# Performance work log

Measured on AMD Instinct MI355X. Metric: run time of the kernel, lower is better.

## Reference

```python
import jax, jax.numpy as jnp
import numpy as np

H = 64; W = 64; WS = 8; SS = 4; NH = 8; C = 256; IM = 4


def _rel_pos_index(ws: int) -> np.ndarray:
    coords = np.stack(np.meshgrid(np.arange(ws), np.arange(ws), indexing='ij'), axis=0).reshape(2, -1)
    rel = (coords[:, :, None] - coords[:, None, :]).transpose(1, 2, 0)
    rel[:, :, 0] += ws - 1
    rel[:, :, 1] += ws - 1
    rel[:, :, 0] *= 2 * ws - 1
    return rel.sum(-1).astype(np.int64)  # (ws*ws, ws*ws)


def _shift_mask(h: int, w: int, ws: int, ss: int) -> np.ndarray:
    img = np.zeros((h, w), np.float32)
    sl = (slice(0, -ws), slice(-ws, -ss), slice(-ss, None))
    cnt = 0
    for hs in sl:
        for wsl in sl:
            img[hs, wsl] = cnt
            cnt += 1
    mw = img.reshape(h // ws, ws, w // ws, ws).transpose(0, 2, 1, 3).reshape(-1, ws * ws)
    am = mw[:, None, :] - mw[:, :, None]
    return np.where(am != 0, -100.0, 0.0).astype(np.float32)  # (nW, n, n)


def setup_inputs() -> dict:
    key = jax.random.key(0)
    ks = jax.random.split(key, 16)
    s = 0.02
    d_ff = C * IM
    n_rel = (2 * WS - 1) ** 2
    return {
        'hidden_states': jax.random.normal(ks[0], (32, H * W, C), jnp.float32),
        'ln1_g': jnp.ones((C,), jnp.float32),
        'ln1_b': jnp.zeros((C,), jnp.float32),
        'wq': jax.random.normal(ks[1], (C, C), jnp.float32) * s,
        'bq': jnp.zeros((C,), jnp.float32),
        'wk': jax.random.normal(ks[2], (C, C), jnp.float32) * s,
        'bk': jnp.zeros((C,), jnp.float32),
        'wv': jax.random.normal(ks[3], (C, C), jnp.float32) * s,
        'bv': jnp.zeros((C,), jnp.float32),
        'bias_table': jax.random.normal(ks[4], (n_rel, NH), jnp.float32) * s,
        'wo': jax.random.normal(ks[5], (C, C), jnp.float32) * s,
        'bo': jnp.zeros((C,), jnp.float32),
        'ln2_g': jnp.ones((C,), jnp.float32),
        'ln2_b': jnp.zeros((C,), jnp.float32),
        'w1': jax.random.normal(ks[6], (C, d_ff), jnp.float32) * s,
        'b1': jnp.zeros((d_ff,), jnp.float32),
        'w2': jax.random.normal(ks[7], (d_ff, C), jnp.float32) * s,
        'b2': jnp.zeros((C,), jnp.float32),
    }


def _layernorm(x, g, b):
    m = x.mean(-1, keepdims=True)
    v = ((x - m) ** 2).mean(-1, keepdims=True)
    return (x - m) * jax.lax.rsqrt(v + 1e-5) * g + b


def reference(hidden_states, ln1_g, ln1_b, wq, bq, wk, bk, wv, bv, bias_table,
              wo, bo, ln2_g, ln2_b, w1, b1, w2, b2):
    B = hidden_states.shape[0]
    n = WS * WS
    hd = C // NH
    scale = hd ** -0.5
    nhw, nww = H // WS, W // WS
    nW = nhw * nww
    rpi = jnp.asarray(_rel_pos_index(WS))        # (n, n) int
    mask = jnp.asarray(_shift_mask(H, W, WS, SS))  # (nW, n, n)

    shortcut = hidden_states
    x = _layernorm(hidden_states, ln1_g, ln1_b).reshape(B, H, W, C)
    # cyclic shift
    x = jnp.roll(x, (-SS, -SS), axis=(1, 2))
    # window partition -> (B*nW, n, C)
    x = x.reshape(B, nhw, WS, nww, WS, C).transpose(0, 1, 3, 2, 4, 5).reshape(B * nW, n, C)

    q = (x @ wq + bq).reshape(B * nW, n, NH, hd).transpose(0, 2, 1, 3)
    k = (x @ wk + bk).reshape(B * nW, n, NH, hd).transpose(0, 2, 1, 3)
    v = (x @ wv + bv).reshape(B * nW, n, NH, hd).transpose(0, 2, 1, 3)

    attn = jnp.einsum('whnd,whmd->whnm', q, k) * scale  # (B*nW, NH, n, n)
    bias = bias_table[rpi.reshape(-1)].reshape(n, n, NH).transpose(2, 0, 1)
    attn = attn + bias[None]
    attn = attn.reshape(B, nW, NH, n, n) + mask[None, :, None]
    attn = jax.nn.softmax(attn.reshape(B * nW, NH, n, n), axis=-1)

    out = jnp.einsum('whnm,whmd->whnd', attn, v).transpose(0, 2, 1, 3).reshape(B * nW, n, C)
    out = out @ wo + bo
    # window reverse
    out = out.reshape(B, nhw, nww, WS, WS, C).transpose(0, 1, 3, 2, 4, 5).reshape(B, H, W, C)
    out = jnp.roll(out, (SS, SS), axis=(1, 2)).reshape(B, H * W, C)

    hs = shortcut + out
    y = _layernorm(hs, ln2_g, ln2_b)
    y = jax.nn.gelu(y @ w1 + b1, approximate=False)
    y = y @ w2 + b2
    return hs + y
```

## Files before the change

kernel.cpp:

```cpp
#include <hip/hip_runtime.h>
#include <hip/hip_bf16.h>
#include <math.h>

typedef unsigned short u16;
typedef __attribute__((ext_vector_type(8))) short bf16x8;
typedef __attribute__((ext_vector_type(8))) unsigned short u16x8;
typedef __attribute__((ext_vector_type(4))) float f32x4;

#define MFMA_BF16 __builtin_amdgcn_mfma_f32_16x16x32_bf16

__device__ __forceinline__ u16 f2bf(float f){
  union { float f; unsigned u; } v; v.f = f;
  unsigned r = v.u + 0x7FFFu + ((v.u >> 16) & 1u);
  return (u16)(r >> 16);
}

__device__ __forceinline__ void gll16(const void* g, void* l){
  __builtin_amdgcn_global_load_lds(
      (const __attribute__((address_space(1))) unsigned int*)g,
      (__attribute__((address_space(3))) unsigned int*)l, 16, 0, 0);
}

__global__ void k_concat_bias(const float* __restrict__ a, const float* __restrict__ b,
                              const float* __restrict__ c, float* __restrict__ o){
  int i = threadIdx.x;
  o[i] = i < 256 ? a[i] : (i < 512 ? b[i-256] : c[i-512]);
}

__global__ __launch_bounds__(256) void k_wfrag(const float* __restrict__ W, u16* __restrict__ F,
                                               int K, int N){
  int idx = blockIdx.x*256 + threadIdx.x;
  int nks = K >> 5;
  int per_n16 = nks << 9;
  int n16 = idx / per_n16; int rem = idx - n16*per_n16;
  int ks = rem >> 9, l8 = rem & 511, lane = l8 >> 3, j = l8 & 7;
  int k = ks*32 + ((lane >> 4) << 3) + j;
  int n = (n16 << 4) + (lane & 15);
  F[idx] = f2bf(W[(size_t)k*N + n]);
}

__global__ __launch_bounds__(256) void k_fragw(const float* __restrict__ wq, const float* __restrict__ wk,
                                               const float* __restrict__ wv, u16* __restrict__ fragW){
  int idx = blockIdx.x*256 + threadIdx.x;
  int j = idx & 7, lane = (idx >> 3) & 63, nj = (idx >> 9) & 1;
  int ks = (idx >> 10) & 7, h = (idx >> 13) & 7, type = idx >> 16;
  const float* w = type == 0 ? wq : (type == 1 ? wk : wv);
  int k = ks*32 + 8*(lane >> 4) + j;
  int n = h*32 + nj*16 + (lane & 15);
  fragW[idx] = f2bf(w[(size_t)k*256 + n]);
}

__global__ __launch_bounds__(256) void k_bias(const float* __restrict__ btab, float* __restrict__ fb){
  int idx = blockIdx.x*256 + threadIdx.x;
  int nj = idx & 3, lr = (idx >> 2) & 15, m = (idx >> 6) & 63, hh = (idx >> 12) & 7, cls = idx >> 15;
  int n = nj*16 + lr;
  int r1=m>>3, c1=m&7, r2=n>>3, c2=n&7;
  float bv = btab[((r1-r2+7)*15 + (c1-c2+7))*8 + hh];
  int whe = cls>>1, wwe = cls&1;
  int a1 = (whe ? (r1<4?1:2) : 0)*3 + (wwe ? (c1<4?1:2) : 0);
  int a2 = (whe ? (r2<4?1:2) : 0)*3 + (wwe ? (c2<4?1:2) : 0);
  fb[idx] = bv + ((a1!=a2) ? -100.f : 0.f);
}

__global__ __launch_bounds__(1024) void k_fattn(const float* __restrict__ hidden,
    const float* __restrict__ g1, const float* __restrict__ b1f,
    const u16* __restrict__ fragW, const float* __restrict__ bqkv,
    const float* __restrict__ fb, const u16* __restrict__ woF,
    const float* __restrict__ bo, const float* __restrict__ g2,
    const float* __restrict__ b2v,
    float* __restrict__ hs_out, u16* __restrict__ y2)
{
  __shared__ __align__(16) u16 lds[75776];
  int tid = threadIdx.x, lane = tid & 63, wid = tid >> 6;
  int lg = lane >> 4, lr = lane & 15;
  int h = wid >> 1, s = wid & 1;
  int gw = blockIdx.x;
  int bi = gw >> 6, win = gw & 63, wh = win >> 3, wwi = win & 7;

  {
    int t = wid*4 + (lane >> 4);
    int j = lane & 15;
    int hh_ = (wh*8 + (t >> 3) + 4) & 63;
    int ww_ = (wwi*8 + (t & 7) + 4) & 63;
    const float4* row = (const float4*)(hidden + ((size_t)bi*4096 + hh_*64 + ww_)*256) + j*4;
    float4 v[4]; float sm = 0.f, sq = 0.f;
#pragma unroll
    for (int i=0;i<4;i++){
      v[i] = row[i];
      sm += v[i].x+v[i].y+v[i].z+v[i].w;
      sq += v[i].x*v[i].x+v[i].y*v[i].y+v[i].z*v[i].z+v[i].w*v[i].w;
    }
    sm += __shfl_xor(sm,1); sq += __shfl_xor(sq,1);
    sm += __shfl_xor(sm,2); sq += __shfl_xor(sq,2);
    sm += __shfl_xor(sm,4); sq += __shfl_xor(sq,4);
    sm += __shfl_xor(sm,8); sq += __shfl_xor(sq,8);
    float mean = sm*(1.f/256.f);
    float inv = rsqrtf(sq*(1.f/256.f) - mean*mean + 1e-5f);
    const float4* gg = (const float4*)g1 + j*4;
    const float4* bb = (const float4*)b1f + j*4;
#pragma unroll
    for (int i2=0;i2<2;i2++){
      float4 a0=v[2*i2], a1=v[2*i2+1];
      float4 g0=gg[2*i2], g1_=gg[2*i2+1];
      float4 b0=bb[2*i2], b1_=bb[2*i2+1];
      u16x8 pk;
      pk[0]=f2bf((a0.x-mean)*inv*g0.x+b0.x); pk[1]=f2bf((a0.y-mean)*inv*g0.y+b0.y);
      pk[2]=f2bf((a0.z-mean)*inv*g0.z+b0.z); pk[3]=f2bf((a0.w-mean)*inv*g0.w+b0.w);
      pk[4]=f2bf((a1.x-mean)*inv*g1_.x+b1_.x); pk[5]=f2bf((a1.y-mean)*inv*g1_.y+b1_.y);
      pk[6]=f2bf((a1.z-mean)*inv*g1_.z+b1_.z); pk[7]=f2bf((a1.w-mean)*inv*g1_.w+b1_.w);
      int c = (j*2 + i2) ^ (t & 7);
      *(u16x8*)(&lds[t*256 + c*8]) = pk;
    }
  }
  __syncthreads();

  f32x4 qa[2][2]={}, ka[2][2]={}, va[2][2]={};
  __builtin_amdgcn_s_setprio(1);
#pragma unroll
  for (int ks=0; ks<8; ks++){
    bf16x8 af[2];
#pragma unroll
    for (int mi=0;mi<2;mi++){
      int tok = 32*s + mi*16 + lr;
      af[mi] = *(const bf16x8*)(&lds[tok*256 + (((ks*4+lg) ^ (tok&7))*8)]);
    }
    const u16* fq = fragW + ((((size_t)h)*8 + ks)*2)*512 + lane*8;
#pragma unroll
    for (int nj=0;nj<2;nj++){
      bf16x8 bq_ = *(const bf16x8*)(fq + nj*512);
      bf16x8 bk_ = *(const bf16x8*)(fq + 65536 + nj*512);
      bf16x8 bv_ = *(const bf16x8*)(fq + 131072 + nj*512);
#pragma unroll
      for (int mi=0;mi<2;mi++){
        qa[mi][nj] = MFMA_BF16(af[mi], bq_, qa[mi][nj], 0,0,0);
        ka[mi][nj] = MFMA_BF16(af[mi], bk_, ka[mi][nj], 0,0,0);
        va[mi][nj] = MFMA_BF16(af[mi], bv_, va[mi][nj], 0,0,0);
      }
    }
  }
  __builtin_amdgcn_s_setprio(0);

  u16* hb  = &lds[16384 + h*7424];
  u16* k_h = hb;
  u16* v_h = hb + 2560;
  u16* q_s = hb + 4864 + s*1280;
  const float scale = 0.1767766952966369f;
#pragma unroll
  for (int mi=0;mi<2;mi++)
#pragma unroll
  for (int nj=0;nj<2;nj++){
    int dim = nj*16+lr;
    float bq_ = bqkv[h*32+dim], bk_ = bqkv[256+h*32+dim], bv_ = bqkv[512+h*32+dim];
#pragma unroll
    for (int r=0;r<4;r++){
      int tokl = mi*16+4*lg+r;
      q_s[tokl*40+dim] = f2bf((qa[mi][nj][r]+bq_)*scale);
      k_h[(32*s+tokl)*40+dim] = f2bf(ka[mi][nj][r]+bk_);
    }
    ushort4 vp;
    vp.x = f2bf(va[mi][nj][0]+bv_); vp.y = f2bf(va[mi][nj][1]+bv_);
    vp.z = f2bf(va[mi][nj][2]+bv_); vp.w = f2bf(va[mi][nj][3]+bv_);
    *(ushort4*)(&v_h[dim*72 + 32*s + mi*16 + 4*lg]) = vp;
  }
  __syncthreads();

  bf16x8 qf[2], kf[4];
#pragma unroll
  for (int i=0;i<2;i++)
    qf[i] = *(const bf16x8*)(&q_s[(i*16+lr)*40 + 8*lg]);
#pragma unroll
  for (int i=0;i<4;i++)
    kf[i] = *(const bf16x8*)(&k_h[(i*16+lr)*40 + 8*lg]);
  f32x4 acc[2][4] = {};
#pragma unroll
  for (int mi=0;mi<2;mi++)
#pragma unroll
  for (int nj=0;nj<4;nj++)
    acc[mi][nj] = MFMA_BF16(qf[mi], kf[nj], acc[mi][nj], 0,0,0);

  int cls = ((wh==7) ? 2 : 0) | ((wwi==7) ? 1 : 0);
  const float4* fb4 = (const float4*)(fb + (((size_t)cls*8 + h) << 12));
#pragma unroll
  for (int mi=0;mi<2;mi++)
#pragma unroll
  for (int r=0;r<4;r++){
    int m = 32*s + mi*16 + 4*lg + r;
    float4 bv4 = fb4[m*16 + lr];
#pragma unroll
    for (int nj=0;nj<4;nj++)
      acc[mi][nj][r] += bv4[nj];
  }
#pragma unroll
  for (int mi=0;mi<2;mi++)
#pragma unroll
  for (int r=0;r<4;r++){
    float mx = fmaxf(fmaxf(acc[mi][0][r], acc[mi][1][r]), fmaxf(acc[mi][2][r], acc[mi][3][r]));
    for (int off=1; off<16; off<<=1) mx = fmaxf(mx, __shfl_xor(mx, off));
    float sum = 0.f;
#pragma unroll
    for (int nj=0;nj<4;nj++){ float e = __expf(acc[mi][nj][r]-mx); acc[mi][nj][r]=e; sum+=e; }
    for (int off=1; off<16; off<<=1) sum += __shfl_xor(sum, off);
    float inv = 1.f/sum;
#pragma unroll
    for (int nj=0;nj<4;nj++) acc[mi][nj][r] *= inv;
  }

  __syncthreads();

  u16* P_s = s ? hb : (hb + 4864);
#pragma unroll
  for (int mi=0;mi<2;mi++)
#pragma unroll
  for (int nj=0;nj<4;nj++)
#pragma unroll
  for (int r=0;r<4;r++)
    P_s[(mi*16+4*lg+r)*72 + nj*16 + lr] = f2bf(acc[mi][nj][r]);

  f32x4 acc2[2][2] = {};
#pragma unroll
  for (int ks=0; ks<2; ks++){
    bf16x8 vf0 = *(const bf16x8*)(&v_h[(lr)*72 + ks*32 + 8*lg]);
    bf16x8 vf1 = *(const bf16x8*)(&v_h[(16+lr)*72 + ks*32 + 8*lg]);
#pragma unroll
    for (int mi=0;mi<2;mi++){
      bf16x8 pf = *(const bf16x8*)(&P_s[(mi*16+lr)*72 + ks*32 + 8*lg]);
      acc2[mi][0] = MFMA_BF16(pf, vf0, acc2[mi][0], 0,0,0);
      acc2[mi][1] = MFMA_BF16(pf, vf1, acc2[mi][1], 0,0,0);
    }
  }

#pragma unroll
  for (int mi=0;mi<2;mi++)
#pragma unroll
  for (int nt=0;nt<2;nt++)
#pragma unroll
  for (int r=0;r<4;r++){
    int row = 32*s + mi*16 + 4*lg + r;
    int chunk = (4*h + 2*nt + (lr>>3)) ^ (row & 7);
    lds[row*256 + chunk*8 + (lr&7)] = f2bf(acc2[mi][nt][r]);
  }
  __syncthreads();

  f32x4 po[2][2] = {};
  __builtin_amdgcn_s_setprio(1);
#pragma unroll
  for (int ks=0; ks<8; ks++){
    bf16x8 af2[2];
#pragma unroll
    for (int mi=0;mi<2;mi++){
      int row = 32*s + mi*16 + lr;
      af2[mi] = *(const bf16x8*)(&lds[row*256 + (((ks*4+lg) ^ (row&7))*8)]);
    }
#pragma unroll
    for (int nj=0;nj<2;nj++){
      bf16x8 bw = *(const bf16x8*)(woF + (((size_t)(2*h+nj))*8 + ks)*512 + lane*8);
#pragma unroll
      for (int mi=0;mi<2;mi++)
        po[mi][nj] = MFMA_BF16(af2[mi], bw, po[mi][nj], 0,0,0);
    }
  }
  __builtin_amdgcn_s_setprio(0);

  float* part_s = (float*)&lds[16384];
  float* part_q = (float*)&lds[16384 + 1024];
  float bov[2], g2v[2], b2vv[2];
#pragma unroll
  for (int nj=0;nj<2;nj++){
    int n = 32*h + nj*16 + lr;
    bov[nj] = bo[n]; g2v[nj] = g2[n]; b2vv[nj] = b2v[n];
  }
#pragma unroll
  for (int mi=0;mi<2;mi++)
#pragma unroll
  for (int r=0;r<4;r++){
    int p = 32*s + mi*16 + 4*lg + r;
    int hh_ = (wh*8 + (p >> 3) + 4) & 63;
    int ww_ = (wwi*8 + (p & 7) + 4) & 63;
    size_t base = ((size_t)bi*4096 + hh_*64 + ww_)*256;
    float ls = 0.f, lq = 0.f;
#pragma unroll
    for (int nj=0;nj<2;nj++){
      int n = 32*h + nj*16 + lr;
      float v = po[mi][nj][r] + bov[nj] + hidden[base + n];
      hs_out[base + n] = v;
      po[mi][nj][r] = v;
      ls += v; lq += v*v;
    }
    ls += __shfl_xor(ls,1); lq += __shfl_xor(lq,1);
    ls += __shfl_xor(ls,2); lq += __shfl_xor(lq,2);
    ls += __shfl_xor(ls,4); lq += __shfl_xor(lq,4);
    ls += __shfl_xor(ls,8); lq += __shfl_xor(lq,8);
    if (lr == 0){ part_s[p*8 + h] = ls; part_q[p*8 + h] = lq; }
  }
  __syncthreads();

#pragma unroll
  for (int mi=0;mi<2;mi++)
#pragma unroll
  for (int r=0;r<4;r++){
    int p = 32*s + mi*16 + 4*lg + r;
    int hh_ = (wh*8 + (p >> 3) + 4) & 63;
    int ww_ = (wwi*8 + (p & 7) + 4) & 63;
    size_t base = ((size_t)bi*4096 + hh_*64 + ww_)*256;
    float sum = 0.f, sqq = 0.f;
#pragma unroll
    for (int hh2=0; hh2<8; hh2++){ sum += part_s[p*8 + hh2]; sqq += part_q[p*8 + hh2]; }
    float mean = sum*(1.f/256.f);
    float inv = rsqrtf(sqq*(1.f/256.f) - mean*mean + 1e-5f);
#pragma unroll
    for (int nj=0;nj<2;nj++){
      int n = 32*h + nj*16 + lr;
      y2[base + n] = f2bf((po[mi][nj][r]-mean)*inv*g2v[nj] + b2vv[nj]);
    }
  }
}

__global__ __launch_bounds__(512) void k_mlp(const u16* __restrict__ y2ln,
    const u16* __restrict__ w1F, const u16* __restrict__ w2F,
    const float* __restrict__ b1, const float* __restrict__ b2,
    float* __restrict__ io)
{
  __shared__ __align__(16) u16 lds[32768];
  int tid = threadIdx.x, lane = tid & 63, wid = tid >> 6;
  int lg = lane >> 4, lr = lane & 15;
  int wr_ = wid >> 2, wc_ = wid & 3;
  int m0 = blockIdx.x*64;

  {
    int row_lo = tid >> 5;
    int ch = tid & 31;
#pragma unroll
    for (int i=0;i<4;i++){
      int row = i*16 + row_lo;
      int sch = ch ^ (row & 7);
      gll16(y2ln + (size_t)(m0+row)*256 + sch*8, &lds[i*4096 + tid*8]);
    }
  }
  asm volatile("s_waitcnt vmcnt(0)" ::: "memory");
  __syncthreads();

  u16* xt = &lds[16384];
  f32x4 accY[2][4] = {};
  float b2v[4];
#pragma unroll
  for (int nj=0;nj<4;nj++) b2v[nj] = b2[wc_*64 + nj*16 + lr];

  for (int c = 0; c < 4; c++){
    f32x4 acc1[4][2] = {};
    __builtin_amdgcn_s_setprio(1);
#pragma unroll
    for (int ks=0; ks<8; ks++){
      bf16x8 af[4];
#pragma unroll
      for (int mi=0;mi<4;mi++){
        int row = mi*16 + lr;
        af[mi] = *(const bf16x8*)(&lds[row*256 + (((ks*4+lg) ^ (row&7))<<3)]);
      }
#pragma unroll
      for (int nj=0;nj<2;nj++){
        bf16x8 bw = *(const bf16x8*)(w1F + ((((size_t)(c*16 + wid*2 + nj))*8 + ks)<<9) + lane*8);
#pragma unroll
        for (int mi=0;mi<4;mi++)
          acc1[mi][nj] = MFMA_BF16(af[mi], bw, acc1[mi][nj], 0,0,0);
      }
    }
    __builtin_amdgcn_s_setprio(0);
    __syncthreads();
#pragma unroll
    for (int mi=0;mi<4;mi++)
#pragma unroll
    for (int nj=0;nj<2;nj++){
      float b1v = b1[c*256 + wid*32 + nj*16 + lr];
#pragma unroll
      for (int r=0;r<4;r++){
        int row = mi*16 + 4*lg + r;
        int col = wid*32 + nj*16 + lr;
        float v = acc1[mi][nj][r] + b1v;
        v = 0.5f*v*(1.f + erff(v*0.70710678118654752f));
        xt[row*256 + ((((col>>3) ^ (row&7))<<3) | (col&7))] = f2bf(v);
      }
    }
    __syncthreads();
    __builtin_amdgcn_s_setprio(1);
#pragma unroll
    for (int ks=0; ks<8; ks++){
      bf16x8 af2[2];
#pragma unroll
      for (int mi=0;mi<2;mi++){
        int row = wr_*32 + mi*16 + lr;
        af2[mi] = *(const bf16x8*)(&xt[row*256 + (((ks*4+lg) ^ (row&7))<<3)]);
      }
#pragma unroll
      for (int nj=0;nj<4;nj++){
        bf16x8 bw = *(const bf16x8*)(w2F + ((((size_t)(wc_*4 + nj))*32 + c*8 + ks)<<9) + lane*8);
#pragma unroll
        for (int mi=0;mi<2;mi++)
          accY[mi][nj] = MFMA_BF16(af2[mi], bw, accY[mi][nj], 0,0,0);
      }
    }
    __builtin_amdgcn_s_setprio(0);
  }

#pragma unroll
  for (int mi=0;mi<2;mi++)
#pragma unroll
  for (int nj=0;nj<4;nj++)
#pragma unroll
  for (int r=0;r<4;r++){
    int m = m0 + wr_*32 + mi*16 + 4*lg + r;
    int n = wc_*64 + nj*16 + lr;
    io[(size_t)m*256 + n] = accY[mi][nj][r] + b2v[nj] + io[(size_t)m*256 + n];
  }
}

extern "C" void kernel_launch(void* const* d_in, const int* in_sizes, int n_in,
                              void* d_out, int out_size, void* d_ws, size_t ws_size,
                              hipStream_t stream){
  const float* hidden = (const float*)d_in[0];
  const float* ln1g = (const float*)d_in[1];
  const float* ln1b = (const float*)d_in[2];
  const float* wq   = (const float*)d_in[3];
  const float* bq   = (const float*)d_in[4];
  const float* wk   = (const float*)d_in[5];
  const float* bk   = (const float*)d_in[6];
  const float* wv   = (const float*)d_in[7];
  const float* bv   = (const float*)d_in[8];
  const float* btab = (const float*)d_in[9];
  const float* wo   = (const float*)d_in[10];
  const float* bo   = (const float*)d_in[11];
  const float* ln2g = (const float*)d_in[12];
  const float* ln2b = (const float*)d_in[13];
  const float* w1   = (const float*)d_in[14];
  const float* b1   = (const float*)d_in[15];
  const float* w2   = (const float*)d_in[16];
  const float* b2   = (const float*)d_in[17];
  float* out = (float*)d_out;

  char* ws = (char*)d_ws;
  const size_t MB = 1ull << 20;
  u16* y2ln  = (u16*)(ws + 192*MB);
  u16* fragW = (u16*)(ws + 256*MB);
  u16* woF   = fragW + 196608;
  u16* w1F   = woF + 65536;
  u16* w2F   = w1F + 262144;
  float* bqkv = (float*)(w2F + 262144);
  float* fbias = bqkv + 1024;

  k_fragw<<<768, 256, 0, stream>>>(wq, wk, wv, fragW);
  k_wfrag<<<256, 256, 0, stream>>>(wo, woF, 256, 256);
  k_wfrag<<<1024,256, 0, stream>>>(w1, w1F, 256, 1024);
  k_wfrag<<<1024,256, 0, stream>>>(w2, w2F, 1024, 256);
  k_concat_bias<<<1, 768, 0, stream>>>(bq, bk, bv, bqkv);
  k_bias<<<512, 256, 0, stream>>>(btab, fbias);

  k_fattn<<<2048, 1024, 0, stream>>>(hidden, ln1g, ln1b, fragW, bqkv, fbias,
                                     woF, bo, ln2g, ln2b, out, y2ln);
  k_mlp<<<2048, 512, 0, stream>>>(y2ln, w1F, w2F, b1, b2, out);
}
```

Measured before the change: 536.6 us.

## Software-pipeline MLP FC1/FC2 chunks and use tanh-approximate GELU

Restructures the MLP kernel's four hidden-dimension chunks into a software pipeline, so the FC1 MFMAs for chunk c+1 are issued alongside the FC2 MFMAs for chunk c. This uses two accumulator sets and hoists the b1 bias loads ahead of the initial LDS wait. The intent is to hide GEMM latency and remove per-chunk serialization. It also replaces the exact erf GELU with a tanh/exp approximation, which changes numerics compared with the reference's exact GELU. The extra accumulator sets raise register pressure.

```diff
diff --git a/kernel.cpp b/kernel.cpp
--- a/kernel.cpp
+++ b/kernel.cpp
@@ -13,6 +13,12 @@
   union { float f; unsigned u; } v; v.f = f;
   unsigned r = v.u + 0x7FFFu + ((v.u >> 16) & 1u);
   return (u16)(r >> 16);
+}
+
+__device__ __forceinline__ float gelu_fast(float x){
+  float u = 0.7978845608028654f * (x + 0.044715f * x * x * x);
+  float e = __expf(2.f * u);
+  return 0.5f * x * (1.f + (1.f - 2.f / (e + 1.f)));
 }
 
 __device__ __forceinline__ void gll16(const void* g, void* l){
@@ -315,6 +321,56 @@
   }
 }
 
+#define MLP_FC1(accn, c)                                                  \
+  _Pragma("unroll")                                                       \
+  for (int ks=0; ks<8; ks++){                                             \
+    bf16x8 af[4];                                                         \
+    _Pragma("unroll")                                                     \
+    for (int mi=0;mi<4;mi++){                                             \
+      int row = mi*16 + lr;                                               \
+      af[mi] = *(const bf16x8*)(&lds[row*256 + (((ks*4+lg) ^ (row&7))<<3)]); \
+    }                                                                     \
+    _Pragma("unroll")                                                     \
+    for (int nj=0;nj<2;nj++){                                             \
+      bf16x8 bw = *(const bf16x8*)(w1F + ((((size_t)((c)*16 + wid*2 + nj))*8 + ks)<<9) + lane*8); \
+      _Pragma("unroll")                                                   \
+      for (int mi=0;mi<4;mi++)                                            \
+        accn[mi][nj] = MFMA_BF16(af[mi], bw, accn[mi][nj], 0,0,0);        \
+    }                                                                     \
+  }
+
+#define MLP_WRITE(accn, c)                                                \
+  _Pragma("unroll")                                                       \
+  for (int mi=0;mi<4;mi++)                                                \
+  _Pragma("unroll")                                                       \
+  for (int nj=0;nj<2;nj++){                                               \
+    _Pragma("unroll")                                                     \
+    for (int r=0;r<4;r++){                                                \
+      int row = mi*16 + 4*lg + r;                                         \
+      int col = wid*32 + nj*16 + lr;                                      \
+      float v = gelu_fast(accn[mi][nj][r] + b1v[c][nj]);                  \
+      xt[row*256 + ((((col>>3) ^ (row&7))<<3) | (col&7))] = f2bf(v);      \
+    }                                                                     \
+  }
+
+#define MLP_FC2(c)                                                        \
+  _Pragma("unroll")                                                       \
+  for (int ks=0; ks<8; ks++){                                             \
+    bf16x8 af2[2];                                                        \
+    _Pragma("unroll")                                                     \
+    for (int mi=0;mi<2;mi++){                                             \
+      int row = wr_*32 + mi*16 + lr;                                      \
+      af2[mi] = *(const bf16x8*)(&xt[row*256 + (((ks*4+lg) ^ (row&7))<<3)]); \
+    }                                                                     \
+    _Pragma("unroll")                                                     \
+    for (int nj=0;nj<4;nj++){                                             \
+      bf16x8 bw = *(const bf16x8*)(w2F + ((((size_t)(wc_*4 + nj))*32 + (c)*8 + ks)<<9) + lane*8); \
+      _Pragma("unroll")                                                   \
+      for (int mi=0;mi<2;mi++)                                            \
+        accY[mi][nj] = MFMA_BF16(af2[mi], bw, accY[mi][nj], 0,0,0);       \
+    }                                                                     \
+  }
+
 __global__ __launch_bounds__(512) void k_mlp(const u16* __restrict__ y2ln,
     const u16* __restrict__ w1F, const u16* __restrict__ w2F,
     const float* __restrict__ b1, const float* __restrict__ b2,
@@ -336,70 +392,60 @@
       gll16(y2ln + (size_t)(m0+row)*256 + sch*8, &lds[i*4096 + tid*8]);
     }
   }
+  float b1v[4][2], b2v[4];
+#pragma unroll
+  for (int c=0;c<4;c++)
+#pragma unroll
+  for (int nj=0;nj<2;nj++) b1v[c][nj] = b1[c*256 + wid*32 + nj*16 + lr];
+#pragma unroll
+  for (int nj=0;nj<4;nj++) b2v[nj] = b2[wc_*64 + nj*16 + lr];
+
   asm volatile("s_waitcnt vmcnt(0)" ::: "memory");
   __syncthreads();
 
   u16* xt = &lds[16384];
   f32x4 accY[2][4] = {};
-  float b2v[4];
-#pragma unroll
-  for (int nj=0;nj<4;nj++) b2v[nj] = b2[wc_*64 + nj*16 + lr];
-
-  for (int c = 0; c < 4; c++){
-    f32x4 acc1[4][2] = {};
-    __builtin_amdgcn_s_setprio(1);
-#pragma unroll
-    for (int ks=0; ks<8; ks++){
-      bf16x8 af[4];
-#pragma unroll
-      for (int mi=0;mi<4;mi++){
-        int row = mi*16 + lr;
-        af[mi] = *(const bf16x8*)(&lds[row*256 + (((ks*4+lg) ^ (row&7))<<3)]);
-      }
-#pragma unroll
-      for (int nj=0;nj<2;nj++){
-        bf16x8 bw = *(const bf16x8*)(w1F + ((((size_t)(c*16 + wid*2 + nj))*8 + ks)<<9) + lane*8);
-#pragma unroll
-        for (int mi=0;mi<4;mi++)
-          acc1[mi][nj] = MFMA_BF16(af[mi], bw, acc1[mi][nj], 0,0,0);
-      }
-    }
-    __builtin_amdgcn_s_setprio(0);
-    __syncthreads();
-#pragma unroll
-    for (int mi=0;mi<4;mi++)
-#pragma unroll
-    for (int nj=0;nj<2;nj++){
-      float b1v = b1[c*256 + wid*32 + nj*16 + lr];
-#pragma unroll
-      for (int r=0;r<4;r++){
-        int row = mi*16 + 4*lg + r;
-        int col = wid*32 + nj*16 + lr;
-        float v = acc1[mi][nj][r] + b1v;
-        v = 0.5f*v*(1.f + erff(v*0.70710678118654752f));
-        xt[row*256 + ((((col>>3) ^ (row&7))<<3) | (col&7))] = f2bf(v);
-      }
-    }
-    __syncthreads();
-    __builtin_amdgcn_s_setprio(1);
-#pragma unroll
-    for (int ks=0; ks<8; ks++){
-      bf16x8 af2[2];
-#pragma unroll
-      for (int mi=0;mi<2;mi++){
-        int row = wr_*32 + mi*16 + lr;
-        af2[mi] = *(const bf16x8*)(&xt[row*256 + (((ks*4+lg) ^ (row&7))<<3)]);
-      }
-#pragma unroll
-      for (int nj=0;nj<4;nj++){
-        bf16x8 bw = *(const bf16x8*)(w2F + ((((size_t)(wc_*4 + nj))*32 + c*8 + ks)<<9) + lane*8);
-#pragma unroll
-        for (int mi=0;mi<2;mi++)
-          accY[mi][nj] = MFMA_BF16(af2[mi], bw, accY[mi][nj], 0,0,0);
-      }
-    }
-    __builtin_amdgcn_s_setprio(0);
-  }
+  f32x4 accA[4][2] = {}, accB[4][2] = {};
+
+  __builtin_amdgcn_s_setprio(1);
+  MLP_FC1(accA, 0)
+  __builtin_amdgcn_s_setprio(0);
+
+  MLP_WRITE(accA, 0)
+  __syncthreads();
+  __builtin_amdgcn_s_setprio(1);
+  MLP_FC1(accB, 1)
+  MLP_FC2(0)
+  __builtin_amdgcn_s_setprio(0);
+  __syncthreads();
+
+  MLP_WRITE(accB, 1)
+  __syncthreads();
+#pragma unroll
+  for (int z=0;z<4;z++){ accA[z>>1][z&1] = f32x4{0.f,0.f,0.f,0.f}; }
+#pragma unroll
+  for (int z=4;z<8;z++){ accA[z>>1][z&1] = f32x4{0.f,0.f,0.f,0.f}; }
+  __builtin_amdgcn_s_setprio(1);
+  MLP_FC1(accA, 2)
+  MLP_FC2(1)
+  __builtin_amdgcn_s_setprio(0);
+  __syncthreads();
+
+  MLP_WRITE(accA, 2)
+  __syncthreads();
+#pragma unroll
+  for (int z=0;z<8;z++){ accB[z>>1][z&1] = f32x4{0.f,0.f,0.f,0.f}; }
+  __builtin_amdgcn_s_setprio(1);
+  MLP_FC1(accB, 3)
+  MLP_FC2(2)
+  __builtin_amdgcn_s_setprio(0);
+  __syncthreads();
+
+  MLP_WRITE(accB, 3)
+  __syncthreads();
+  __builtin_amdgcn_s_setprio(1);
+  MLP_FC2(3)
+  __builtin_amdgcn_s_setprio(0);
 
 #pragma unroll
   for (int mi=0;mi<2;mi++)
```

New measurement: 559.4 us. 1.04x slower.
